# Performance work log

Hardware: AMD Instinct MI355X
Metric: run time of the kernel (lower is better)

## Reference

```python
import jax, jax.numpy as jnp
import numpy as np

B, N, D, H = 32, 64, 128, 256
LN_EPS = 1e-5


def _mlp(x, W1, b1, g, beta, W2, b2):
    # Linear -> LayerNorm -> GELU (exact erf) -> Linear
    h = x @ W1 + b1
    mu = jnp.mean(h, axis=-1, keepdims=True)
    var = jnp.var(h, axis=-1, keepdims=True)
    h = (h - mu) * jax.lax.rsqrt(var + LN_EPS) * g + beta
    h = jax.nn.gelu(h, approximate=False)
    return h @ W2 + b2


def setup_inputs() -> dict:
    key = jax.random.key(0)
    ks = jax.random.split(key, 10)
    s = lambda fan_in: 1.0 / np.sqrt(fan_in)
    return {
        "slots": jax.random.normal(ks[0], (B, N, D), dtype=jnp.float32),
        "adjacency": jax.random.uniform(ks[1], (B, N, N), dtype=jnp.float32),
        # edge_net params
        "We1": jax.random.uniform(ks[2], (2 * D, H), minval=-s(2 * D), maxval=s(2 * D), dtype=jnp.float32),
        "be1": jnp.zeros((H,), jnp.float32),
        "ge": jnp.ones((H,), jnp.float32),
        "bge": jnp.zeros((H,), jnp.float32),
        "We2": jax.random.uniform(ks[3], (H, D), minval=-s(H), maxval=s(H), dtype=jnp.float32),
        "be2": jnp.zeros((D,), jnp.float32),
        # node_net params
        "Wn1": jax.random.uniform(ks[4], (2 * D, H), minval=-s(2 * D), maxval=s(2 * D), dtype=jnp.float32),
        "bn1": jnp.zeros((H,), jnp.float32),
        "gn": jnp.ones((H,), jnp.float32),
        "bgn": jnp.zeros((H,), jnp.float32),
        "Wn2": jax.random.uniform(ks[5], (H, D), minval=-s(H), maxval=s(H), dtype=jnp.float32),
        "bn2": jnp.zeros((D,), jnp.float32),
    }


def reference(slots, adjacency, We1, be1, ge, bge, We2, be2, Wn1, bn1, gn, bgn, Wn2, bn2):
    b, n, d = slots.shape
    # all-pairs edge features: receiver i, sender j -> [B,N,N,2D]
    ei = jnp.broadcast_to(slots[:, :, None, :], (b, n, n, d))
    ej = jnp.broadcast_to(slots[:, None, :, :], (b, n, n, d))
    edge_feat = jnp.concatenate([ei, ej], axis=-1)
    edge_out = _mlp(edge_feat, We1, be1, ge, bge, We2, be2)  # [B,N,N,D]
    # mask diagonal (i != j) and weight by adjacency, then reduce over j
    mask = 1.0 - jnp.eye(n, dtype=slots.dtype)
    w = adjacency * mask  # [B,N,N]
    messages = jnp.einsum('bij,bijd->bid', w, edge_out)
    node_input = jnp.concatenate([slots, messages], axis=-1)
    delta = _mlp(node_input, Wn1, bn1, gn, bgn, Wn2, bn2)
    return slots + delta
```

## Files before the change

### kernel.cpp

```cpp
#include <hip/hip_runtime.h>

#define NB 32
#define NN 64
#define ND 128
#define NH 256
#define LN_EPS 1e-5f
#define RP 4

typedef __attribute__((ext_vector_type(8))) short bf16x8;
typedef __attribute__((ext_vector_type(4))) float f32x4;

__device__ __forceinline__ float gelu2(float x) {
    const float au  = fabsf(x);
    const float xpa = x + au;
    const float z   = au * 0.70710678118654752440f;
    const float z2  = z * z;
    const float pc  = fmaf(0.078108f, z, 0.000972f);
    const float pb  = fmaf(0.278393f, z, 1.0f);
    const float p   = fmaf(z2, fmaf(z, pc, 0.230389f), pb);
    const float p2  = p * p;
    const float r   = __builtin_amdgcn_rcpf(p2 * p2);
    return fmaf(-au, r, xpa);
}
__device__ __forceinline__ float gelu_h(float x) { return 0.5f * gelu2(x); }

__device__ __forceinline__ short f2bf(float f) {
    unsigned u = __float_as_uint(f);
    u += 0x7FFFu + ((u >> 16) & 1u);
    return (short)(u >> 16);
}
__device__ __forceinline__ float bflo(unsigned u) { return __uint_as_float(u << 16); }
__device__ __forceinline__ float bfhi(unsigned u) { return __uint_as_float(u & 0xFFFF0000u); }

__global__ __launch_bounds__(256) void k_pre(const float* __restrict__ slots,
                                             const float* __restrict__ We1,
                                             const float* __restrict__ be1,
                                             const float* __restrict__ Wn1,
                                             const float* __restrict__ We2,
                                             const float* __restrict__ be2,
                                             const float* __restrict__ Wn2,
                                             float* __restrict__ Pt,
                                             float* __restrict__ Qm,
                                             float* __restrict__ XW,
                                             short* __restrict__ Pb,
                                             short* __restrict__ Qb,
                                             float4* __restrict__ rowstats,
                                             unsigned short* __restrict__ WCb,
                                             float* __restrict__ v,
                                             unsigned short* __restrict__ Wn2b) {
    __shared__ float xs[RP][ND];
    __shared__ float red[4][RP][4];
    const int t = threadIdx.x;

    if (blockIdx.x >= 512) {
        const int bid2 = blockIdx.x - 512;
        if (bid2 == 64) {
            __shared__ float bs[ND];
            if (t < ND) bs[t] = be2[t];
            __syncthreads();
            float acc = 0.f;
            #pragma unroll 4
            for (int d = 0; d < ND; ++d) acc = fmaf(bs[d], Wn1[(ND + d) * NH + t], acc);
            v[t] = acc;
            return;
        }
        if (bid2 > 64) {
            const int base = (bid2 - 65) * 8192;
            #pragma unroll 8
            for (int i = 0; i < 32; ++i) {
                const int idx = base + i * 256 + t;
                Wn2b[idx] = (unsigned short)f2bf(Wn2[idx]);
            }
            return;
        }
        const int k0 = bid2 * 4;
        __shared__ float ws[4][ND];
        #pragma unroll
        for (int i = 0; i < 2; ++i) {
            const int idx = t + i * 256;
            ws[idx >> 7][idx & 127] = We2[(k0 + (idx >> 7)) * ND + (idx & 127)];
        }
        __syncthreads();
        float acc[4] = {0.f, 0.f, 0.f, 0.f};
        #pragma unroll 4
        for (int d = 0; d < ND; ++d) {
            const float wn = Wn1[(ND + d) * NH + t];
            #pragma unroll
            for (int r = 0; r < 4; ++r) acc[r] = fmaf(ws[r][d], wn, acc[r]);
        }
        #pragma unroll
        for (int r = 0; r < 4; ++r)
            WCb[(size_t)(k0 + r) * NH + t] = (unsigned short)f2bf(acc[r]);
        return;
    }

    const int r0 = blockIdx.x * RP;
    const int lane = t & 63, wave = t >> 6;
    #pragma unroll
    for (int i = 0; i < 2; ++i) {
        const int idx = t + i * 256;
        xs[idx >> 7][idx & 127] = slots[(size_t)(r0 + (idx >> 7)) * ND + (idx & 127)];
    }
    __syncthreads();
    float pt[RP], qq[RP], xw[RP];
    const float bb = be1[t];
    #pragma unroll
    for (int r = 0; r < RP; ++r) { pt[r] = bb; qq[r] = 0.f; xw[r] = 0.f; }
    #pragma unroll 4
    for (int d = 0; d < ND; ++d) {
        const float wt  = We1[d * NH + t];
        const float wbt = We1[(ND + d) * NH + t];
        const float wn  = Wn1[d * NH + t];
        #pragma unroll
        for (int r = 0; r < RP; ++r) {
            const float x = xs[r][d];
            pt[r] = fmaf(x, wt,  pt[r]);
            qq[r] = fmaf(x, wbt, qq[r]);
            xw[r] = fmaf(x, wn,  xw[r]);
        }
    }
    #pragma unroll
    for (int r = 0; r < RP; ++r) {
        const size_t row = (size_t)(r0 + r);
        Pt[row * NH + t] = pt[r];
        Qm[row * NH + t] = qq[r];
        XW[row * NH + t] = xw[r];
        Pb[row * NH + t] = f2bf(pt[r]);
        Qb[row * NH + t] = f2bf(qq[r]);
    }
    float s1[RP], s2[RP], s3[RP], s4[RP];
    #pragma unroll
    for (int r = 0; r < RP; ++r) {
        s1[r] = pt[r]; s2[r] = pt[r] * pt[r];
        s3[r] = qq[r]; s4[r] = qq[r] * qq[r];
    }
    #pragma unroll
    for (int off = 32; off; off >>= 1) {
        #pragma unroll
        for (int r = 0; r < RP; ++r) {
            s1[r] += __shfl_xor(s1[r], off);
            s2[r] += __shfl_xor(s2[r], off);
            s3[r] += __shfl_xor(s3[r], off);
            s4[r] += __shfl_xor(s4[r], off);
        }
    }
    if (lane == 0) {
        #pragma unroll
        for (int r = 0; r < RP; ++r) {
            red[wave][r][0] = s1[r]; red[wave][r][1] = s2[r];
            red[wave][r][2] = s3[r]; red[wave][r][3] = s4[r];
        }
    }
    __syncthreads();
    if (t < RP) {
        float4 st;
        st.x = (red[0][t][0] + red[1][t][0]) + (red[2][t][0] + red[3][t][0]);
        st.y = (red[0][t][1] + red[1][t][1]) + (red[2][t][1] + red[3][t][1]);
        st.z = (red[0][t][2] + red[1][t][2]) + (red[2][t][2] + red[3][t][2]);
        st.w = (red[0][t][3] + red[1][t][3]) + (red[2][t][3] + red[3][t][3]);
        rowstats[r0 + t] = st;
    }
}

__global__ __launch_bounds__(256) void k_dot(
    const short* __restrict__ Pb, const short* __restrict__ Qb,
    const float4* __restrict__ rowstats,
    const float* __restrict__ adj,
    float4* __restrict__ wmrG)
{
    const int b  = blockIdx.x >> 2;
    const int jt = blockIdx.x & 3;
    const int t  = threadIdx.x;
    const int l  = t & 63;
    const int i0 = (t >> 6) * 16;
    const int j0 = jt * 16;
    const int rA = l & 15;
    const int kg = l >> 4;

    const short* Prow = Pb + ((size_t)b * NN + i0 + rA) * NH + kg * 8;
    const short* Qrow = Qb + ((size_t)b * NN + j0 + rA) * NH + kg * 8;
    f32x4 acc = {0.f, 0.f, 0.f, 0.f};
    #pragma unroll
    for (int kc = 0; kc < 8; ++kc) {
        const bf16x8 av = *(const bf16x8*)(Prow + kc * 32);
        const bf16x8 bv = *(const bf16x8*)(Qrow + kc * 32);
        acc = __builtin_amdgcn_mfma_f32_16x16x32_bf16(av, bv, acc, 0, 0, 0);
    }
    const int j  = j0 + rA;
    const int gj = b * NN + j;
    const float4 stj = rowstats[gj];
    const float inv = 1.0f / NH;
    #pragma unroll
    for (int q = 0; q < 4; ++q) {
        const int i  = i0 + kg * 4 + q;
        const int gi = b * NN + i;
        const float4 sti = rowstats[gi];
        float a = adj[(size_t)gi * NN + j];
        if (j == i) a = 0.f;
        const float cd = acc[q];
        const float mu = (sti.x + stj.z) * inv;
        const float e2 = fmaf(2.f, cd, sti.y + stj.w) * inv;
        const float rr = __builtin_amdgcn_rsqf(fmaf(-mu, mu, e2) + LN_EPS);
        wmrG[(size_t)gi * NN + j] = make_float4(0.5f * a, rr, -mu * rr, a);
    }
}

__global__ __launch_bounds__(256, 4) void k_mn(
    const float* __restrict__ slots,
    const float* __restrict__ Pt,
    const float* __restrict__ Qm,
    const float4* __restrict__ wmrG,
    const float* __restrict__ ge,  const float* __restrict__ bge,
    const float* __restrict__ XW,
    const unsigned short* __restrict__ WCb, const float* __restrict__ v,
    const float* __restrict__ bn1,
    const float* __restrict__ gn,  const float* __restrict__ bgn,
    const unsigned short* __restrict__ Wn2b, const float* __restrict__ bn2,
    float* __restrict__ out)
{
    union U {
        struct { float4 wmr[2][NN]; float s[4][2][NH]; } e;
        struct { float sfg[2][NH];
                 union { float part[2][4][NH]; float d[2][8][ND + 4]; } w; } n;
    };
    __shared__ U u;
    __shared__ float lds_ws[2];
    __shared__ float lds_red[4][2][2];
    __shared__ float lds_mr[2][2];

    const int row0 = blockIdx.x * 2;
    const int b    = row0 >> 6;
    const int t    = threadIdx.x;
    const int lane = t & 63;
    const int wave = t >> 6;

    const float xw0 = XW[(size_t)row0 * NH + t];
    const float xw1 = XW[(size_t)(row0 + 1) * NH + t];
    const float sl  = slots[(size_t)(row0 + (t >> 7)) * ND + (t & 127)];
    if (t < 128) {
        const int r = t >> 6, j = t & 63;
        u.e.wmr[r][j] = wmrG[(size_t)(row0 + r) * NN + j];
    }
    const float4 P0 = ((const float4*)(Pt + (size_t)row0 * NH))[lane];
    const float4 P1 = ((const float4*)(Pt + (size_t)(row0 + 1) * NH))[lane];
    const float4 G  = ((const float4*)ge)[lane];
    const float4 Bg = ((const float4*)bge)[lane];
    __syncthreads();

    if (wave < 2) {
        float wv = u.e.wmr[wave][lane].w;
        #pragma unroll
        for (int off = 32; off; off >>= 1) wv += __shfl_xor(wv, off);
        if (lane == 0) lds_ws[wave] = wv;
    }

    const float4* Qb4 = (const float4*)(Qm + (size_t)b * NN * NH) + lane;
    float4 A0 = make_float4(0.f, 0.f, 0.f, 0.f);
    float4 A1 = make_float4(0.f, 0.f, 0.f, 0.f);
    #pragma unroll 4
    for (int k = 0; k < 16; ++k) {
        const int jj = wave + 4 * k;
        const float4 q  = Qb4[jj * (NH / 4)];
        const float4 m0 = u.e.wmr[0][jj];
        const float4 m1 = u.e.wmr[1][jj];
        float h, uu;
        h = P0.x + q.x; uu = fmaf(fmaf(h, m0.y, m0.z), G.x, Bg.x); A0.x = fmaf(m0.x, gelu2(uu), A0.x);
        h = P0.y + q.y; uu = fmaf(fmaf(h, m0.y, m0.z), G.y, Bg.y); A0.y = fmaf(m0.x, gelu2(uu), A0.y);
        h = P0.z + q.z; uu = fmaf(fmaf(h, m0.y, m0.z), G.z, Bg.z); A0.z = fmaf(m0.x, gelu2(uu), A0.z);
        h = P0.w + q.w; uu = fmaf(fmaf(h, m0.y, m0.z), G.w, Bg.w); A0.w = fmaf(m0.x, gelu2(uu), A0.w);
        h = P1.x + q.x; uu = fmaf(fmaf(h, m1.y, m1.z), G.x, Bg.x); A1.x = fmaf(m1.x, gelu2(uu), A1.x);
        h = P1.y + q.y; uu = fmaf(fmaf(h, m1.y, m1.z), G.y, Bg.y); A1.y = fmaf(m1.x, gelu2(uu), A1.y);
        h = P1.z + q.z; uu = fmaf(fmaf(h, m1.y, m1.z), G.z, Bg.z); A1.z = fmaf(m1.x, gelu2(uu), A1.z);
        h = P1.w + q.w; uu = fmaf(fmaf(h, m1.y, m1.z), G.w, Bg.w); A1.w = fmaf(m1.x, gelu2(uu), A1.w);
    }
    ((float4*)u.e.s[wave][0])[lane] = A0;
    ((float4*)u.e.s[wave][1])[lane] = A1;
    __syncthreads();

    const float sf0 = (u.e.s[0][0][t] + u.e.s[1][0][t]) + (u.e.s[2][0][t] + u.e.s[3][0][t]);
    const float sf1 = (u.e.s[0][1][t] + u.e.s[1][1][t]) + (u.e.s[2][1][t] + u.e.s[3][1][t]);
    __syncthreads();
    u.n.sfg[0][t] = sf0;
    u.n.sfg[1][t] = sf1;
    __syncthreads();

    {
        const int ks = wave;
        const int cg = lane;
        float4 h0 = make_float4(0.f, 0.f, 0.f, 0.f);
        float4 h1 = make_float4(0.f, 0.f, 0.f, 0.f);
        const uint2* wc2 = (const uint2*)WCb + cg;
        #pragma unroll 8
        for (int k = ks * 64; k < ks * 64 + 64; ++k) {
            const uint2 wp = wc2[k * 64];
            const float w0 = bflo(wp.x), w1 = bfhi(wp.x);
            const float w2v = bflo(wp.y), w3 = bfhi(wp.y);
            const float sa = u.n.sfg[0][k];
            const float sb = u.n.sfg[1][k];
            h0.x = fmaf(sa, w0, h0.x); h0.y = fmaf(sa, w1, h0.y);
            h0.z = fmaf(sa, w2v, h0.z); h0.w = fmaf(sa, w3, h0.w);
            h1.x = fmaf(sb, w0, h1.x); h1.y = fmaf(sb, w1, h1.y);
            h1.z = fmaf(sb, w2v, h1.z); h1.w = fmaf(sb, w3, h1.w);
        }
        ((float4*)u.n.w.part[0][ks])[cg] = h0;
        ((float4*)u.n.w.part[1][ks])[cg] = h1;
    }
    __syncthreads();

    float a0, a1;
    {
        const float b1 = bn1[t], vc = v[t];
        a0 = (u.n.w.part[0][0][t] + u.n.w.part[0][1][t])
           + (u.n.w.part[0][2][t] + u.n.w.part[0][3][t])
           + fmaf(lds_ws[0], vc, b1) + xw0;
        a1 = (u.n.w.part[1][0][t] + u.n.w.part[1][1][t])
           + (u.n.w.part[1][2][t] + u.n.w.part[1][3][t])
           + fmaf(lds_ws[1], vc, b1) + xw1;
    }
    {
        float s1 = a0, s2 = a0 * a0, s3 = a1, s4 = a1 * a1;
        #pragma unroll
        for (int off = 32; off; off >>= 1) {
            s1 += __shfl_xor(s1, off); s2 += __shfl_xor(s2, off);
            s3 += __shfl_xor(s3, off); s4 += __shfl_xor(s4, off);
        }
        if (lane == 0) {
            lds_red[wave][0][0] = s1; lds_red[wave][0][1] = s2;
            lds_red[wave][1][0] = s3; lds_red[wave][1][1] = s4;
        }
    }
    __syncthreads();
    if (t < 2) {
        const float S1 = (lds_red[0][t][0] + lds_red[1][t][0]) + (lds_red[2][t][0] + lds_red[3][t][0]);
        const float S2 = (lds_red[0][t][1] + lds_red[1][t][1]) + (lds_red[2][t][1] + lds_red[3][t][1]);
        const float mu  = S1 * (1.0f / NH);
        const float var = fmaf(-mu, mu, S2 * (1.0f / NH));
        lds_mr[t][0] = mu;
        lds_mr[t][1] = __builtin_amdgcn_rsqf(var + LN_EPS);
    }
    __syncthreads();
    {
        const float g = gn[t], bg = bgn[t];
        const float rr0 = lds_mr[0][1], rr1 = lds_mr[1][1];
        u.n.sfg[0][t] = gelu_h(fmaf(fmaf(a0, rr0, -lds_mr[0][0] * rr0), g, bg));
        u.n.sfg[1][t] = gelu_h(fmaf(fmaf(a1, rr1, -lds_mr[1][0] * rr1), g, bg));
    }
    __syncthreads();

    {
        const int ks = t >> 5;
        const int cg = t & 31;
        float4 d0 = make_float4(0.f, 0.f, 0.f, 0.f);
        float4 d1 = make_float4(0.f, 0.f, 0.f, 0.f);
        const uint2* w2b = (const uint2*)Wn2b + cg;
        const int kbeg = ks * 32;
        #pragma unroll 8
        for (int k = kbeg; k < kbeg + 32; ++k) {
            const uint2 wp = w2b[k * 32];
            const float w0 = bflo(wp.x), w1 = bfhi(wp.x);
            const float w2v = bflo(wp.y), w3 = bfhi(wp.y);
            const float g0 = u.n.sfg[0][k];
            const float g1 = u.n.sfg[1][k];
            d0.x = fmaf(g0, w0, d0.x); d0.y = fmaf(g0, w1, d0.y);
            d0.z = fmaf(g0, w2v, d0.z); d0.w = fmaf(g0, w3, d0.w);
            d1.x = fmaf(g1, w0, d1.x); d1.y = fmaf(g1, w1, d1.y);
            d1.z = fmaf(g1, w2v, d1.z); d1.w = fmaf(g1, w3, d1.w);
        }
        ((float4*)u.n.w.d[0][ks])[cg] = d0;
        ((float4*)u.n.w.d[1][ks])[cg] = d1;
    }
    __syncthreads();
    {
        const int r  = t >> 7;
        const int c2 = t & 127;
        float ds = 0.f;
        #pragma unroll
        for (int p2 = 0; p2 < 8; ++p2) ds += u.n.w.d[r][p2][c2];
        out[(size_t)(row0 + r) * ND + c2] = sl + bn2[c2] + ds;
    }
}

extern "C" void kernel_launch(void* const* d_in, const int* in_sizes, int n_in,
                              void* d_out, int out_size, void* d_ws, size_t ws_size,
                              hipStream_t stream) {
    const float* slots = (const float*)d_in[0];
    const float* adj   = (const float*)d_in[1];
    const float* We1   = (const float*)d_in[2];
    const float* be1   = (const float*)d_in[3];
    const float* ge    = (const float*)d_in[4];
    const float* bge   = (const float*)d_in[5];
    const float* We2   = (const float*)d_in[6];
    const float* be2   = (const float*)d_in[7];
    const float* Wn1   = (const float*)d_in[8];
    const float* bn1   = (const float*)d_in[9];
    const float* gn    = (const float*)d_in[10];
    const float* bgn   = (const float*)d_in[11];
    const float* Wn2   = (const float*)d_in[12];
    const float* bn2   = (const float*)d_in[13];
    float* out = (float*)d_out;

    const size_t RN = (size_t)NB * NN;
    float*  Ptw  = (float*)d_ws;
    float*  Qw   = Ptw  + RN * NH;
    float*  XWw  = Qw   + RN * NH;
    float*  vw   = XWw  + RN * NH;
    float4* rsw  = (float4*)(vw + NH + 768);
    float4* wmrw = rsw + RN;
    short*  Pbw  = (short*)(wmrw + RN * NN);
    short*  Qbw  = Pbw + RN * NH;
    unsigned short* WCbw  = (unsigned short*)(Qbw + RN * NH);
    unsigned short* Wn2bw = WCbw + (size_t)NH * NH;

    k_pre<<<581,            256, 0, stream>>>(slots, We1, be1, Wn1, We2, be2, Wn2,
                                              Ptw, Qw, XWw, Pbw, Qbw, rsw, WCbw, vw, Wn2bw);
    k_dot<<<NB * 4,         256, 0, stream>>>(Pbw, Qbw, rsw, adj, wmrw);
    k_mn <<<(int)(RN / 2),  256, 0, stream>>>(slots, Ptw, Qw, wmrw, ge, bge,
                                              XWw, WCbw, vw, bn1, gn, bgn, Wn2bw, bn2, out);
}
```

Before: 55.06 us.

## Double k_mn block to 512 threads, one row per half-block

```diff
diff --git a/kernel.cpp b/kernel.cpp
--- a/kernel.cpp
+++ b/kernel.cpp
@@ -205,7 +205,7 @@
     }
 }
 
-__global__ __launch_bounds__(256, 4) void k_mn(
+__global__ __launch_bounds__(512, 8) void k_mn(
     const float* __restrict__ slots,
     const float* __restrict__ Pt,
     const float* __restrict__ Qm,
@@ -219,13 +219,14 @@
     float* __restrict__ out)
 {
     union U {
-        struct { float4 wmr[2][NN]; float s[4][2][NH]; } e;
+        struct { float4 wmr[2][NN]; float s[8][NH]; } e;
         struct { float sfg[2][NH];
-                 union { float part[2][4][NH]; float d[2][8][ND + 4]; } w; } n;
+                 union { float part[8][2][NH];
+                         float d[2][16][ND + 4]; } w; } n;
     };
     __shared__ U u;
     __shared__ float lds_ws[2];
-    __shared__ float lds_red[4][2][2];
+    __shared__ float lds_red[8][2];
     __shared__ float lds_mr[2][2];
 
     const int row0 = blockIdx.x * 2;
@@ -233,16 +234,16 @@
     const int t    = threadIdx.x;
     const int lane = t & 63;
     const int wave = t >> 6;
-
-    const float xw0 = XW[(size_t)row0 * NH + t];
-    const float xw1 = XW[(size_t)(row0 + 1) * NH + t];
-    const float sl  = slots[(size_t)(row0 + (t >> 7)) * ND + (t & 127)];
-    if (t < 128) {
-        const int r = t >> 6, j = t & 63;
-        u.e.wmr[r][j] = wmrG[(size_t)(row0 + r) * NN + j];
-    }
-    const float4 P0 = ((const float4*)(Pt + (size_t)row0 * NH))[lane];
-    const float4 P1 = ((const float4*)(Pt + (size_t)(row0 + 1) * NH))[lane];
+    const int half = t >> 8;
+    const int c    = t & 255;
+    const int wih  = wave & 3;
+
+    const int myrow = row0 + half;
+    const float xw = XW[(size_t)myrow * NH + c];
+    float sl = 0.f;
+    if (t < 256) sl = slots[(size_t)(row0 + (t >> 7)) * ND + (t & 127)];
+    if (t < 128) u.e.wmr[t >> 6][t & 63] = wmrG[(size_t)(row0 + (t >> 6)) * NN + (t & 63)];
+    const float4 P  = ((const float4*)(Pt + (size_t)myrow * NH))[lane];
     const float4 G  = ((const float4*)ge)[lane];
     const float4 Bg = ((const float4*)bge)[lane];
     __syncthreads();
@@ -255,33 +256,24 @@
     }
 
     const float4* Qb4 = (const float4*)(Qm + (size_t)b * NN * NH) + lane;
-    float4 A0 = make_float4(0.f, 0.f, 0.f, 0.f);
-    float4 A1 = make_float4(0.f, 0.f, 0.f, 0.f);
+    float4 A = make_float4(0.f, 0.f, 0.f, 0.f);
     #pragma unroll 4
     for (int k = 0; k < 16; ++k) {
-        const int jj = wave + 4 * k;
-        const float4 q  = Qb4[jj * (NH / 4)];
-        const float4 m0 = u.e.wmr[0][jj];
-        const float4 m1 = u.e.wmr[1][jj];
+        const int jj = wih + 4 * k;
+        const float4 q = Qb4[jj * (NH / 4)];
+        const float4 m = u.e.wmr[half][jj];
         float h, uu;
-        h = P0.x + q.x; uu = fmaf(fmaf(h, m0.y, m0.z), G.x, Bg.x); A0.x = fmaf(m0.x, gelu2(uu), A0.x);
-        h = P0.y + q.y; uu = fmaf(fmaf(h, m0.y, m0.z), G.y, Bg.y); A0.y = fmaf(m0.x, gelu2(uu), A0.y);
-        h = P0.z + q.z; uu = fmaf(fmaf(h, m0.y, m0.z), G.z, Bg.z); A0.z = fmaf(m0.x, gelu2(uu), A0.z);
-        h = P0.w + q.w; uu = fmaf(fmaf(h, m0.y, m0.z), G.w, Bg.w); A0.w = fmaf(m0.x, gelu2(uu), A0.w);
-        h = P1.x + q.x; uu = fmaf(fmaf(h, m1.y, m1.z), G.x, Bg.x); A1.x = fmaf(m1.x, gelu2(uu), A1.x);
-        h = P1.y + q.y; uu = fmaf(fmaf(h, m1.y, m1.z), G.y, Bg.y); A1.y = fmaf(m1.x, gelu2(uu), A1.y);
-        h = P1.z + q.z; uu = fmaf(fmaf(h, m1.y, m1.z), G.z, Bg.z); A1.z = fmaf(m1.x, gelu2(uu), A1.z);
-        h = P1.w + q.w; uu = fmaf(fmaf(h, m1.y, m1.z), G.w, Bg.w); A1.w = fmaf(m1.x, gelu2(uu), A1.w);
-    }
-    ((float4*)u.e.s[wave][0])[lane] = A0;
-    ((float4*)u.e.s[wave][1])[lane] = A1;
-    __syncthreads();
-
-    const float sf0 = (u.e.s[0][0][t] + u.e.s[1][0][t]) + (u.e.s[2][0][t] + u.e.s[3][0][t]);
-    const float sf1 = (u.e.s[0][1][t] + u.e.s[1][1][t]) + (u.e.s[2][1][t] + u.e.s[3][1][t]);
-    __syncthreads();
-    u.n.sfg[0][t] = sf0;
-    u.n.sfg[1][t] = sf1;
+        h = P.x + q.x; uu = fmaf(fmaf(h, m.y, m.z), G.x, Bg.x); A.x = fmaf(m.x, gelu2(uu), A.x);
+        h = P.y + q.y; uu = fmaf(fmaf(h, m.y, m.z), G.y, Bg.y); A.y = fmaf(m.x, gelu2(uu), A.y);
+        h = P.z + q.z; uu = fmaf(fmaf(h, m.y, m.z), G.z, Bg.z); A.z = fmaf(m.x, gelu2(uu), A.z);
+        h = P.w + q.w; uu = fmaf(fmaf(h, m.y, m.z), G.w, Bg.w); A.w = fmaf(m.x, gelu2(uu), A.w);
+    }
+    ((float4*)u.e.s[wave])[lane] = A;
+    __syncthreads();
+
+    const float sf = (u.e.s[half * 4 + 0][c] + u.e.s[half * 4 + 1][c])
+                   + (u.e.s[half * 4 + 2][c] + u.e.s[half * 4 + 3][c]);
+    u.n.sfg[half][c] = sf;
     __syncthreads();
 
     {
@@ -291,7 +283,7 @@
         float4 h1 = make_float4(0.f, 0.f, 0.f, 0.f);
         const uint2* wc2 = (const uint2*)WCb + cg;
         #pragma unroll 8
-        for (int k = ks * 64; k < ks * 64 + 64; ++k) {
+        for (int k = ks * 32; k < ks * 32 + 32; ++k) {
             const uint2 wp = wc2[k * 64];
             const float w0 = bflo(wp.x), w1 = bfhi(wp.x);
             const float w2v = bflo(wp.y), w3 = bfhi(wp.y);
@@ -302,37 +294,33 @@
             h1.x = fmaf(sb, w0, h1.x); h1.y = fmaf(sb, w1, h1.y);
             h1.z = fmaf(sb, w2v, h1.z); h1.w = fmaf(sb, w3, h1.w);
         }
-        ((float4*)u.n.w.part[0][ks])[cg] = h0;
-        ((float4*)u.n.w.part[1][ks])[cg] = h1;
-    }
-    __syncthreads();
-
-    float a0, a1;
+        ((float4*)u.n.w.part[ks][0])[cg] = h0;
+        ((float4*)u.n.w.part[ks][1])[cg] = h1;
+    }
+    __syncthreads();
+
+    float a0;
     {
-        const float b1 = bn1[t], vc = v[t];
-        a0 = (u.n.w.part[0][0][t] + u.n.w.part[0][1][t])
-           + (u.n.w.part[0][2][t] + u.n.w.part[0][3][t])
-           + fmaf(lds_ws[0], vc, b1) + xw0;
-        a1 = (u.n.w.part[1][0][t] + u.n.w.part[1][1][t])
-           + (u.n.w.part[1][2][t] + u.n.w.part[1][3][t])
-           + fmaf(lds_ws[1], vc, b1) + xw1;
+        const float b1 = bn1[c], vc = v[c];
+        float sum = 0.f;
+        #pragma unroll
+        for (int p = 0; p < 8; ++p) sum += u.n.w.part[p][half][c];
+        a0 = sum + fmaf(lds_ws[half], vc, b1) + xw;
     }
     {
-        float s1 = a0, s2 = a0 * a0, s3 = a1, s4 = a1 * a1;
+        float s1 = a0, s2 = a0 * a0;
         #pragma unroll
         for (int off = 32; off; off >>= 1) {
             s1 += __shfl_xor(s1, off); s2 += __shfl_xor(s2, off);
-            s3 += __shfl_xor(s3, off); s4 += __shfl_xor(s4, off);
-        }
-        if (lane == 0) {
-            lds_red[wave][0][0] = s1; lds_red[wave][0][1] = s2;
-            lds_red[wave][1][0] = s3; lds_red[wave][1][1] = s4;
-        }
+        }
+        if (lane == 0) { lds_red[wave][0] = s1; lds_red[wave][1] = s2; }
     }
     __syncthreads();
     if (t < 2) {
-        const float S1 = (lds_red[0][t][0] + lds_red[1][t][0]) + (lds_red[2][t][0] + lds_red[3][t][0]);
-        const float S2 = (lds_red[0][t][1] + lds_red[1][t][1]) + (lds_red[2][t][1] + lds_red[3][t][1]);
+        const float S1 = (lds_red[4 * t + 0][0] + lds_red[4 * t + 1][0])
+                       + (lds_red[4 * t + 2][0] + lds_red[4 * t + 3][0]);
+        const float S2 = (lds_red[4 * t + 0][1] + lds_red[4 * t + 1][1])
+                       + (lds_red[4 * t + 2][1] + lds_red[4 * t + 3][1]);
         const float mu  = S1 * (1.0f / NH);
         const float var = fmaf(-mu, mu, S2 * (1.0f / NH));
         lds_mr[t][0] = mu;
@@ -340,22 +328,20 @@
     }
     __syncthreads();
     {
-        const float g = gn[t], bg = bgn[t];
-        const float rr0 = lds_mr[0][1], rr1 = lds_mr[1][1];
-        u.n.sfg[0][t] = gelu_h(fmaf(fmaf(a0, rr0, -lds_mr[0][0] * rr0), g, bg));
-        u.n.sfg[1][t] = gelu_h(fmaf(fmaf(a1, rr1, -lds_mr[1][0] * rr1), g, bg));
+        const float g = gn[c], bg = bgn[c];
+        const float rr = lds_mr[half][1];
+        u.n.sfg[half][c] = gelu_h(fmaf(fmaf(a0, rr, -lds_mr[half][0] * rr), g, bg));
     }
     __syncthreads();
 
     {
-        const int ks = t >> 5;
-        const int cg = t & 31;
+        const int ks2 = t >> 5;
+        const int cg2 = t & 31;
         float4 d0 = make_float4(0.f, 0.f, 0.f, 0.f);
         float4 d1 = make_float4(0.f, 0.f, 0.f, 0.f);
-        const uint2* w2b = (const uint2*)Wn2b + cg;
-        const int kbeg = ks * 32;
+        const uint2* w2b = (const uint2*)Wn2b + cg2;
         #pragma unroll 8
-        for (int k = kbeg; k < kbeg + 32; ++k) {
+        for (int k = ks2 * 16; k < ks2 * 16 + 16; ++k) {
             const uint2 wp = w2b[k * 32];
             const float w0 = bflo(wp.x), w1 = bfhi(wp.x);
             const float w2v = bflo(wp.y), w3 = bfhi(wp.y);
@@ -366,16 +352,16 @@
             d1.x = fmaf(g1, w0, d1.x); d1.y = fmaf(g1, w1, d1.y);
             d1.z = fmaf(g1, w2v, d1.z); d1.w = fmaf(g1, w3, d1.w);
         }
-        ((float4*)u.n.w.d[0][ks])[cg] = d0;
-        ((float4*)u.n.w.d[1][ks])[cg] = d1;
-    }
-    __syncthreads();
-    {
+        ((float4*)u.n.w.d[0][ks2])[cg2] = d0;
+        ((float4*)u.n.w.d[1][ks2])[cg2] = d1;
+    }
+    __syncthreads();
+    if (t < 256) {
         const int r  = t >> 7;
         const int c2 = t & 127;
         float ds = 0.f;
         #pragma unroll
-        for (int p2 = 0; p2 < 8; ++p2) ds += u.n.w.d[r][p2][c2];
+        for (int p = 0; p < 16; ++p) ds += u.n.w.d[r][p][c2];
         out[(size_t)(row0 + r) * ND + c2] = sl + bn2[c2] + ds;
     }
 }
@@ -414,6 +400,6 @@
     k_pre<<<581,            256, 0, stream>>>(slots, We1, be1, Wn1, We2, be2, Wn2,
                                               Ptw, Qw, XWw, Pbw, Qbw, rsw, WCbw, vw, Wn2bw);
     k_dot<<<NB * 4,         256, 0, stream>>>(Pbw, Qbw, rsw, adj, wmrw);
-    k_mn <<<(int)(RN / 2),  256, 0, stream>>>(slots, Ptw, Qw, wmrw, ge, bge,
+    k_mn <<<(int)(RN / 2),  512, 0, stream>>>(slots, Ptw, Qw, wmrw, ge, bge,
                                               XWw, WCbw, vw, bn1, gn, bgn, Wn2bw, bn2, out);
 }
```

Result: slower. 59.71 us (+8.4%).
